# Kernel optimization log

Measured on AMD Instinct MI355X. Metric: run time of the kernel, lower is better.

## Reference

```python
import jax, jax.numpy as jnp
import numpy as np

NEG_SLOPE = 0.2  # PyG GATv2Conv default leaky_relu slope
N_NODES = 50000
N_EDGES = 800000
F_IN = 128
HID = 32
HEADS = 4
OUT_HEADS = 1
N_CLS = 16
MLP_HID = 128


def topk_mask(score, dst, k, num_nodes):
    """Boolean mask [E,H]: True where edge score is among top-k for its destination."""
    E = score.shape[0]
    counts = jnp.zeros((num_nodes,), jnp.int32).at[dst].add(1)
    starts = jnp.cumsum(counts) - counts  # first sorted index of each dst segment

    def one_head(s):
        o1 = jnp.argsort(-s)                       # sort by score desc
        o2 = jnp.argsort(dst[o1], stable=True)     # stable sort by dst -> (dst asc, score desc)
        perm = o1[o2]
        rank = jnp.arange(E) - starts[dst[perm]]   # rank within dst segment
        return jnp.zeros((E,), bool).at[perm].set(rank < k)

    return jax.vmap(one_head, in_axes=1, out_axes=1)(score)


def masked_segment_softmax(score, mask, dst, num_nodes):
    neg = jnp.where(mask, score, -jnp.inf)
    m = jax.ops.segment_max(neg, dst, num_segments=num_nodes)
    m = jnp.where(jnp.isfinite(m), m, 0.0)
    ex = jnp.where(mask, jnp.exp(score - m[dst]), 0.0)
    s = jax.ops.segment_sum(ex, dst, num_segments=num_nodes)
    return ex / (s[dst] + 1e-16)


def gatv2_topk(x, edge_index, k, Wl, Wr, att, b, heads, out_c, concat, num_nodes):
    src, dst = edge_index[0], edge_index[1]
    xl = (x @ Wl).reshape(num_nodes, heads, out_c)
    xr = (x @ Wr).reshape(num_nodes, heads, out_c)
    h = xl[src] + xr[dst]                                   # [E,H,C]
    e = jnp.einsum('ehc,hc->eh', jax.nn.leaky_relu(h, NEG_SLOPE), att)  # [E,H]
    keep = topk_mask(e, dst, k, num_nodes)
    alpha = masked_segment_softmax(e, keep, dst, num_nodes)       # top-k attention
    alpha_n = masked_segment_softmax(e, ~keep, dst, num_nodes)    # truncated (noise) attention
    msg = xl[src]                                                  # [E,H,C]
    out = jax.ops.segment_sum(alpha[..., None] * msg, dst, num_segments=num_nodes)
    noise = jax.ops.segment_sum(alpha_n[..., None] * msg, dst, num_segments=num_nodes)
    if concat:
        out = out.reshape(num_nodes, heads * out_c)
        noise = noise.reshape(num_nodes, heads * out_c)
    else:
        out = out.mean(axis=1)
        noise = noise.mean(axis=1)
    return out + b, noise + b


def setup_inputs() -> dict:
    key = jax.random.key(0)
    ks = jax.random.split(key, 14)
    s = 0.1
    x = jax.random.normal(ks[0], (N_NODES, F_IN), jnp.float32)
    edge_index = jax.random.randint(ks[1], (2, N_EDGES), 0, N_NODES, dtype=jnp.int64)
    return {
        'x': x,
        'edge_index': edge_index,
        'attn_topk': 8,
        'Wl1': jax.random.normal(ks[2], (F_IN, HEADS * HID), jnp.float32) * s,
        'Wr1': jax.random.normal(ks[3], (F_IN, HEADS * HID), jnp.float32) * s,
        'att1': jax.random.normal(ks[4], (HEADS, HID), jnp.float32) * s,
        'b1': jnp.zeros((HEADS * HID,), jnp.float32),
        'Wl2': jax.random.normal(ks[5], (HEADS * HID, OUT_HEADS * N_CLS), jnp.float32) * s,
        'Wr2': jax.random.normal(ks[6], (HEADS * HID, OUT_HEADS * N_CLS), jnp.float32) * s,
        'att2': jax.random.normal(ks[7], (OUT_HEADS, N_CLS), jnp.float32) * s,
        'b2': jnp.zeros((N_CLS,), jnp.float32),
        'lin1_w': jax.random.normal(ks[8], (HEADS * HID, MLP_HID), jnp.float32) * s,
        'lin1_b': jnp.zeros((MLP_HID,), jnp.float32),
        'lin2_w': jax.random.normal(ks[9], (MLP_HID, N_CLS), jnp.float32) * s,
        'lin2_b': jnp.zeros((N_CLS,), jnp.float32),
    }


def reference(x, edge_index, attn_topk, Wl1, Wr1, att1, b1, Wl2, Wr2, att2, b2,
              lin1_w, lin1_b, lin2_w, lin2_b):
    # eval mode: dropout is identity
    h, noise1 = gatv2_topk(x, edge_index, attn_topk, Wl1, Wr1, att1, b1,
                           HEADS, HID, True, N_NODES)
    h = jax.nn.elu(h)
    n1 = jax.nn.elu(noise1 @ lin1_w + lin1_b) @ lin2_w + lin2_b
    out, noise2 = gatv2_topk(h, edge_index, attn_topk, Wl2, Wr2, att2, b2,
                             OUT_HEADS, N_CLS, False, N_NODES)
    return (jax.nn.log_softmax(out, axis=1),
            jax.nn.log_softmax(n1, axis=1),
            jax.nn.log_softmax(noise2, axis=1))
```

## Files before the change

kernel.cpp:

```cpp
#include <hip/hip_runtime.h>
#include <math.h>

#define NN 50000
#define NE 800000
#define FIN 128
#define HEADS 4
#define HID 32
#define D1 128
#define NCLS 16
#define NEG 0.2f
#define NINF (-3.402823466e38f)
#define CAP 64
#define SB 256
#define NSB ((NN + SB - 1) / SB)

typedef unsigned long long ull;
typedef __attribute__((ext_vector_type(8))) short bf16x8;
typedef __attribute__((ext_vector_type(4))) float f32x4;

__device__ __forceinline__ short f2bf(float v) {
  unsigned u = __float_as_uint(v);
  unsigned r = (u + 0x7fffu + ((u >> 16) & 1u)) >> 16;
  return (short)r;
}

__global__ void k_count(const int* __restrict__ dst, int* __restrict__ counts) {
  int j = blockIdx.x * 256 + threadIdx.x;
  if (j < NE) atomicAdd(&counts[dst[j]], 1);
}

__global__ void k_scanA(const int* __restrict__ counts, int* __restrict__ bsum) {
  int b = blockIdx.x, t = threadIdx.x;
  int idx = b * SB + t;
  int v = idx < NN ? counts[idx] : 0;
  __shared__ int ws[4];
#pragma unroll
  for (int o = 1; o <= 32; o <<= 1) v += __shfl_xor(v, o, 64);
  if ((t & 63) == 0) ws[t >> 6] = v;
  __syncthreads();
  if (t == 0) bsum[b] = ws[0] + ws[1] + ws[2] + ws[3];
}

__global__ void k_scanB(const int* __restrict__ bsum, int* __restrict__ boff) {
  int t = threadIdx.x;
  int v = t < NSB ? bsum[t] : 0;
  __shared__ int tmp[256];
  tmp[t] = v;
  __syncthreads();
  for (int o = 1; o < 256; o <<= 1) {
    int u = t >= o ? tmp[t - o] : 0;
    __syncthreads();
    tmp[t] += u;
    __syncthreads();
  }
  if (t < NSB) boff[t] = tmp[t] - v;
}

__global__ void k_scanC(const int* __restrict__ counts, const int* __restrict__ boff,
                        int* __restrict__ starts, int* __restrict__ cursor) {
  int b = blockIdx.x, t = threadIdx.x;
  int idx = b * SB + t;
  int v = idx < NN ? counts[idx] : 0;
  __shared__ int tmp[256];
  tmp[t] = v;
  __syncthreads();
  for (int o = 1; o < 256; o <<= 1) {
    int u = t >= o ? tmp[t - o] : 0;
    __syncthreads();
    tmp[t] += u;
    __syncthreads();
  }
  int ex = tmp[t] - v + boff[b];
  if (idx < NN) { starts[idx] = ex; cursor[idx] = ex; }
}

__global__ void k_scatter(const int* __restrict__ src, const int* __restrict__ dst,
                          int* __restrict__ cursor, int* __restrict__ eperm,
                          int* __restrict__ sperm) {
  int j = blockIdx.x * 256 + threadIdx.x;
  if (j < NE) {
    int p = atomicAdd(&cursor[dst[j]], 1);
    eperm[p] = j;
    sperm[p] = src[j];
  }
}

template <int BM, int BN, int BK, int TM, int TN, int ACT>
__global__ __launch_bounds__(256) void k_gemm2(
    const float* __restrict__ A, const float* __restrict__ B1,
    const float* __restrict__ B2, int N1, int s1, int s2,
    const float* __restrict__ bias, float* __restrict__ C, int M, int N, int K) {
  constexpr int NT = (BM / TM) * (BN / TN);
  static_assert(NT == 256, "block must be 256 threads");
  static_assert(TM % 4 == 0 && TN % 4 == 0, "float4 fragments");
  __shared__ float As[BK][BM + 4];
  __shared__ float Bs[BK][BN];
  int tid = threadIdx.x;
  int bm = blockIdx.y * BM, bn = blockIdx.x * BN;
  constexpr int TX = BN / TN;
  int tn = (tid % TX) * TN;
  int tm = (tid / TX) * TM;
  float acc[TM][TN];
#pragma unroll
  for (int i = 0; i < TM; i++)
#pragma unroll
    for (int j = 0; j < TN; j++) acc[i][j] = 0.f;

  for (int k0 = 0; k0 < K; k0 += BK) {
    constexpr int AV = BM * BK / 4;
    for (int i = tid; i < AV; i += NT) {
      int r = i / (BK / 4);
      int c4 = (i % (BK / 4)) * 4;
      float4 v = make_float4(0.f, 0.f, 0.f, 0.f);
      int gr = bm + r;
      if (gr < M) v = *(const float4*)(A + (size_t)gr * K + k0 + c4);
      As[c4 + 0][r] = v.x; As[c4 + 1][r] = v.y; As[c4 + 2][r] = v.z; As[c4 + 3][r] = v.w;
    }
    constexpr int BV = BK * BN / 4;
    for (int i = tid; i < BV; i += NT) {
      int r = i / (BN / 4), c4 = (i % (BN / 4)) * 4;
      int gc = bn + c4, gk = k0 + r;
      float4 v = (gc < N1) ? *(const float4*)(B1 + (size_t)gk * s1 + gc)
                           : *(const float4*)(B2 + (size_t)gk * s2 + (gc - N1));
      Bs[r][c4 + 0] = v.x; Bs[r][c4 + 1] = v.y; Bs[r][c4 + 2] = v.z; Bs[r][c4 + 3] = v.w;
    }
    __syncthreads();
#pragma unroll
    for (int kk = 0; kk < BK; kk++) {
      float ra[TM], rb[TN];
#pragma unroll
      for (int i = 0; i < TM; i += 4)
        *(float4*)&ra[i] = *(const float4*)&As[kk][tm + i];
#pragma unroll
      for (int j = 0; j < TN; j += 4)
        *(float4*)&rb[j] = *(const float4*)&Bs[kk][tn + j];
#pragma unroll
      for (int i = 0; i < TM; i++)
#pragma unroll
        for (int j = 0; j < TN; j++) acc[i][j] += ra[i] * rb[j];
    }
    __syncthreads();
  }
#pragma unroll
  for (int i = 0; i < TM; i++) {
    int gr = bm + tm + i;
    if (gr >= M) continue;
#pragma unroll
    for (int j = 0; j < TN; j += 4) {
      float4 v;
      v.x = acc[i][j + 0]; v.y = acc[i][j + 1]; v.z = acc[i][j + 2]; v.w = acc[i][j + 3];
      if (bias) {
        v.x += bias[bn + tn + j + 0]; v.y += bias[bn + tn + j + 1];
        v.z += bias[bn + tn + j + 2]; v.w += bias[bn + tn + j + 3];
      }
      if (ACT == 1) {
        v.x = v.x > 0.f ? v.x : expm1f(v.x);
        v.y = v.y > 0.f ? v.y : expm1f(v.y);
        v.z = v.z > 0.f ? v.z : expm1f(v.z);
        v.w = v.w > 0.f ? v.w : expm1f(v.w);
      }
      *(float4*)(C + (size_t)gr * N + bn + tn + j) = v;
    }
  }
}

__global__ void k_cvtw(const float* __restrict__ l1w, const float* __restrict__ l2w,
                       short* __restrict__ w1t, short* __restrict__ w2t) {
  int t = blockIdx.x * 256 + threadIdx.x;
  if (t < 128 * 128) {
    int n = t >> 7, k = t & 127;
    w1t[t] = f2bf(l1w[k * 128 + n]);
  }
  if (t < 16 * 128) {
    int n = t >> 7, k = t & 127;
    w2t[t] = f2bf(l2w[k * 16 + n]);
  }
}

__global__ __launch_bounds__(256) void k_mlp1(
    const short* __restrict__ A, const short* __restrict__ BT,
    const float* __restrict__ bias, short* __restrict__ C) {
  int wv = threadIdx.x >> 6, lane = threadIdx.x & 63;
  int m0 = (blockIdx.x * 4 + wv) * 16;
  int quad = lane >> 4;
  int mr = m0 + (lane & 15);
  bool mok = mr < NN;
  bf16x8 afr[4];
#pragma unroll
  for (int kt = 0; kt < 4; kt++) {
    bf16x8 z = {0, 0, 0, 0, 0, 0, 0, 0};
    afr[kt] = mok ? *(const bf16x8*)(A + (size_t)mr * 128 + kt * 32 + quad * 8) : z;
  }
#pragma unroll
  for (int nt = 0; nt < 8; nt++) {
    f32x4 acc = {0.f, 0.f, 0.f, 0.f};
    int nc = nt * 16 + (lane & 15);
#pragma unroll
    for (int kt = 0; kt < 4; kt++) {
      bf16x8 bfr = *(const bf16x8*)(BT + (size_t)nc * 128 + kt * 32 + quad * 8);
      acc = __builtin_amdgcn_mfma_f32_16x16x32_bf16(afr[kt], bfr, acc, 0, 0, 0);
    }
    float bval = bias[nc];
#pragma unroll
    for (int r = 0; r < 4; r++) {
      int row = m0 + quad * 4 + r;
      if (row < NN) {
        float v = acc[r] + bval;
        v = v > 0.f ? v : expm1f(v);
        C[(size_t)row * 128 + nc] = f2bf(v);
      }
    }
  }
}

__global__ __launch_bounds__(256) void k_mlp2(
    const short* __restrict__ A, const short* __restrict__ BT,
    const float* __restrict__ bias, float* __restrict__ out) {
  int wv = threadIdx.x >> 6, lane = threadIdx.x & 63;
  int m0 = (blockIdx.x * 4 + wv) * 16;
  int quad = lane >> 4, col = lane & 15;
  int mr = m0 + col;
  bool mok = mr < NN;
  f32x4 acc = {0.f, 0.f, 0.f, 0.f};
#pragma unroll
  for (int kt = 0; kt < 4; kt++) {
    bf16x8 z = {0, 0, 0, 0, 0, 0, 0, 0};
    bf16x8 afr = mok ? *(const bf16x8*)(A + (size_t)mr * 128 + kt * 32 + quad * 8) : z;
    bf16x8 bfr = *(const bf16x8*)(BT + (size_t)col * 128 + kt * 32 + quad * 8);
    acc = __builtin_amdgcn_mfma_f32_16x16x32_bf16(afr, bfr, acc, 0, 0, 0);
  }
  float bval = bias[col];
#pragma unroll
  for (int r = 0; r < 4; r++) {
    float v = acc[r] + bval;
    float m = v;
#pragma unroll
    for (int o = 1; o <= 8; o <<= 1) m = fmaxf(m, __shfl_xor(m, o, 64));
    float e = __expf(v - m), s = e;
#pragma unroll
    for (int o = 1; o <= 8; o <<= 1) s += __shfl_xor(s, o, 64);
    int row = m0 + quad * 4 + r;
    if (row < NN) out[(size_t)row * NCLS + col] = v - (m + logf(s));
  }
}

__device__ __forceinline__ unsigned fkey(float f) {
  unsigned u = __float_as_uint(f);
  return u ^ (((int)u >> 31) | 0x80000000u);
}

__global__ __launch_bounds__(256) void k_fused1(
    const float* __restrict__ xlr, const float* __restrict__ att,
    const int* __restrict__ sperm, const int* __restrict__ eperm,
    const int* __restrict__ starts, const int* __restrict__ counts,
    const int* __restrict__ kptr, const float* __restrict__ bias,
    float* __restrict__ hout, short* __restrict__ nout) {
  __shared__ float sc[4][CAP][4];
  __shared__ ull keys[4][4][CAP + 1];
  int w = threadIdx.x >> 6;
  int l = threadIdx.x & 63;
  int d = blockIdx.x * 4 + w;
  if (d >= NN) return;
  int st = starts[d];
  int deg = counts[d];
  if (deg > CAP) deg = CAP;
  int k = kptr[0];

  int srcreg = 0, idreg = 0x7fffffff;
  if (l < deg) { srcreg = sperm[st + l]; idreg = eperm[st + l]; }

  int h2 = l >> 5, li = l & 31;
  int headq = li >> 3;
  float4 xrv = *(const float4*)(xlr + (size_t)d * 256 + 128 + 4 * li);
  float4 attv = *(const float4*)(att + 4 * li);
  float4 b1v = *(const float4*)(bias + 4 * li);

  float4 xc[8];
#pragma unroll
  for (int j = 0; j < 8; j++) xc[j] = make_float4(0.f, 0.f, 0.f, 0.f);

#pragma unroll
  for (int Q = 0; Q < 16; Q += 8) {
    if (Q < deg) {
      int rr[4]; float4 xv[4]; float pp[4]; bool vv[4];
#pragma unroll
      for (int j = 0; j < 4; j++) {
        rr[j] = Q + 2 * j + h2;
        int s = __shfl(srcreg, rr[j]);
        vv[j] = rr[j] < deg;
        xv[j] = make_float4(0.f, 0.f, 0.f, 0.f);
        if (vv[j]) xv[j] = *(const float4*)(xlr + (size_t)s * 256 + 4 * li);
        xc[Q / 2 + j] = xv[j];
      }
#pragma unroll
      for (int j = 0; j < 4; j++) {
        float a, p = 0.f;
        a = xv[j].x + xrv.x; p += fmaxf(a, NEG * a) * attv.x;
        a = xv[j].y + xrv.y; p += fmaxf(a, NEG * a) * attv.y;
        a = xv[j].z + xrv.z; p += fmaxf(a, NEG * a) * attv.z;
        a = xv[j].w + xrv.w; p += fmaxf(a, NEG * a) * attv.w;
        pp[j] = p;
      }
#pragma unroll
      for (int o = 1; o <= 4; o <<= 1) {
#pragma unroll
        for (int j = 0; j < 4; j++) pp[j] += __shfl_xor(pp[j], o, 64);
      }
      if ((li & 7) == 0) {
#pragma unroll
        for (int j = 0; j < 4; j++)
          if (vv[j]) sc[w][rr[j]][headq] = pp[j];
      }
    }
  }
  for (int q = 16; q < deg; q += 8) {
    int rr[4]; float4 xv[4]; float pp[4]; bool vv[4];
#pragma unroll
    for (int j = 0; j < 4; j++) {
      rr[j] = q + 2 * j + h2;
      int s = __shfl(srcreg, rr[j]);
      vv[j] = rr[j] < deg;
      xv[j] = make_float4(0.f, 0.f, 0.f, 0.f);
      if (vv[j]) xv[j] = *(const float4*)(xlr + (size_t)s * 256 + 4 * li);
    }
#pragma unroll
    for (int j = 0; j < 4; j++) {
      float a, p = 0.f;
      a = xv[j].x + xrv.x; p += fmaxf(a, NEG * a) * attv.x;
      a = xv[j].y + xrv.y; p += fmaxf(a, NEG * a) * attv.y;
      a = xv[j].z + xrv.z; p += fmaxf(a, NEG * a) * attv.z;
      a = xv[j].w + xrv.w; p += fmaxf(a, NEG * a) * attv.w;
      pp[j] = p;
    }
#pragma unroll
    for (int o = 1; o <= 4; o <<= 1) {
#pragma unroll
      for (int j = 0; j < 4; j++) pp[j] += __shfl_xor(pp[j], o, 64);
    }
    if ((li & 7) == 0) {
#pragma unroll
      for (int j = 0; j < 4; j++)
        if (vv[j]) sc[w][rr[j]][headq] = pp[j];
    }
  }

  int hh = l >> 4, ii = l & 15;
  float sv[4]; bool val[4]; ull mkey[4]; int rank[4];
#pragma unroll
  for (int j = 0; j < 4; j++) {
    int q = j * 16 + ii;
    val[j] = q < deg;
    sv[j] = val[j] ? sc[w][q][hh] : NINF;
    int bid = __shfl(idreg, q);
    mkey[j] = val[j] ? (((ull)fkey(sv[j]) << 32) | (unsigned)~bid) : 0ull;
    rank[j] = 0;
    if (val[j]) keys[w][hh][q] = mkey[j];
  }
  int nch = (deg + 15) >> 4;
  const ull* kp = keys[w][hh];
  if (nch == 1) {
    int r0 = 0;
    for (int p = 0; p < deg; p++) r0 += kp[p] > mkey[0];
    rank[0] = r0;
  } else if (nch == 2) {
    int r0 = 0, r1 = 0;
    for (int p = 0; p < deg; p++) {
      ull bk = kp[p];
      r0 += bk > mkey[0]; r1 += bk > mkey[1];
    }
    rank[0] = r0; rank[1] = r1;
  } else {
    for (int p = 0; p < deg; p++) {
      ull bk = kp[p];
#pragma unroll
      for (int j = 0; j < 4; j++) rank[j] += bk > mkey[j];
    }
  }
  bool kept[4];
#pragma unroll
  for (int j = 0; j < 4; j++) kept[j] = val[j] && (rank[j] < k);

  float mk = fmaxf(fmaxf(sv[0], sv[1]), fmaxf(sv[2], sv[3]));
  float mn = NINF;
#pragma unroll
  for (int j = 0; j < 4; j++) mn = fmaxf(mn, kept[j] ? NINF : sv[j]);
#pragma unroll
  for (int o = 1; o <= 8; o <<= 1) {
    mk = fmaxf(mk, __shfl_xor(mk, o, 64));
    mn = fmaxf(mn, __shfl_xor(mn, o, 64));
  }
  float ek[4], en[4], sk = 0.f, sn = 0.f;
#pragma unroll
  for (int j = 0; j < 4; j++) {
    ek[j] = kept[j] ? __expf(sv[j] - mk) : 0.f;
    en[j] = (val[j] && !kept[j]) ? __expf(sv[j] - mn) : 0.f;
    sk += ek[j]; sn += en[j];
  }
#pragma unroll
  for (int o = 1; o <= 8; o <<= 1) {
    sk += __shfl_xor(sk, o, 64);
    sn += __shfl_xor(sn, o, 64);
  }
  float ik = 1.f / (sk + 1e-16f), inn = 1.f / (sn + 1e-16f);
#pragma unroll
  for (int j = 0; j < 4; j++) {
    if (val[j]) sc[w][j * 16 + ii][hh] = kept[j] ? ek[j] * ik : -(en[j] * inn);
  }

  float4 ao = make_float4(0.f, 0.f, 0.f, 0.f), an = ao;
#pragma unroll
  for (int j = 0; j < 8; j++) {
    int r = 2 * j + h2;
    if (r < deg) {
      float wv = sc[w][r][headq];
      float pw = fmaxf(wv, 0.f), nw = pw - wv;
      float4 xv = xc[j];
      ao.x += pw * xv.x; ao.y += pw * xv.y; ao.z += pw * xv.z; ao.w += pw * xv.w;
      an.x += nw * xv.x; an.y += nw * xv.y; an.z += nw * xv.z; an.w += nw * xv.w;
    }
  }
  for (int q = 16; q < deg; q += 4) {
    int r0 = q + h2, r1 = q + 2 + h2;
    int s0 = __shfl(srcreg, r0), s1 = __shfl(srcreg, r1);
    if (r0 < deg) {
      float wv = sc[w][r0][headq];
      float pw = fmaxf(wv, 0.f), nw = pw - wv;
      float4 xv = *(const float4*)(xlr + (size_t)s0 * 256 + 4 * li);
      ao.x += pw * xv.x; ao.y += pw * xv.y; ao.z += pw * xv.z; ao.w += pw * xv.w;
      an.x += nw * xv.x; an.y += nw * xv.y; an.z += nw * xv.z; an.w += nw * xv.w;
    }
    if (r1 < deg) {
      float wv = sc[w][r1][headq];
      float pw = fmaxf(wv, 0.f), nw = pw - wv;
      float4 xv = *(const float4*)(xlr + (size_t)s1 * 256 + 4 * li);
      ao.x += pw * xv.x; ao.y += pw * xv.y; ao.z += pw * xv.z; ao.w += pw * xv.w;
      an.x += nw * xv.x; an.y += nw * xv.y; an.z += nw * xv.z; an.w += nw * xv.w;
    }
  }
  ao.x += __shfl_xor(ao.x, 32, 64); ao.y += __shfl_xor(ao.y, 32, 64);
  ao.z += __shfl_xor(ao.z, 32, 64); ao.w += __shfl_xor(ao.w, 32, 64);
  an.x += __shfl_xor(an.x, 32, 64); an.y += __shfl_xor(an.y, 32, 64);
  an.z += __shfl_xor(an.z, 32, 64); an.w += __shfl_xor(an.w, 32, 64);
  if (h2 == 0) {
    float4 vo;
    vo.x = ao.x + b1v.x; vo.y = ao.y + b1v.y; vo.z = ao.z + b1v.z; vo.w = ao.w + b1v.w;
    vo.x = vo.x > 0.f ? vo.x : expm1f(vo.x);
    vo.y = vo.y > 0.f ? vo.y : expm1f(vo.y);
    vo.z = vo.z > 0.f ? vo.z : expm1f(vo.z);
    vo.w = vo.w > 0.f ? vo.w : expm1f(vo.w);
    *(float4*)(hout + (size_t)d * D1 + 4 * li) = vo;
  } else {
    short4 vn;
    vn.x = f2bf(an.x + b1v.x); vn.y = f2bf(an.y + b1v.y);
    vn.z = f2bf(an.z + b1v.z); vn.w = f2bf(an.w + b1v.w);
    *(short4*)(nout + (size_t)d * D1 + 4 * li) = vn;
  }
}

__global__ __launch_bounds__(256) void k_fused2(
    const float* __restrict__ xlr, const float* __restrict__ att,
    const int* __restrict__ sperm, const int* __restrict__ eperm,
    const int* __restrict__ starts, const int* __restrict__ counts,
    const int* __restrict__ kptr, const float* __restrict__ bias,
    float* __restrict__ out0, float* __restrict__ out1) {
  __shared__ float sc[4][CAP];
  __shared__ ull keys[4][CAP];
  int w = threadIdx.x >> 6;
  int l = threadIdx.x & 63;
  int d = blockIdx.x * 4 + w;
  if (d >= NN) return;
  int st = starts[d];
  int deg = counts[d];
  if (deg > CAP) deg = CAP;
  int k = kptr[0];

  int srcreg = 0, idreg = 0x7fffffff;
  if (l < deg) { srcreg = sperm[st + l]; idreg = eperm[st + l]; }

  int g = l >> 4, li = l & 15;
  float xrv = xlr[(size_t)d * 32 + 16 + li];
  float attv = att[li];
  float bv2 = bias[li];

  float xc[8];
#pragma unroll
  for (int j = 0; j < 8; j++) xc[j] = 0.f;

#pragma unroll
  for (int Q = 0; Q < 32; Q += 8) {
    if (Q < deg) {
      int r0 = Q + g, r1 = Q + 4 + g;
      int s0 = __shfl(srcreg, r0), s1 = __shfl(srcreg, r1);
      float x0 = (r0 < deg) ? xlr[(size_t)s0 * 32 + li] : 0.f;
      float x1 = (r1 < deg) ? xlr[(size_t)s1 * 32 + li] : 0.f;
      xc[Q / 4] = x0; xc[Q / 4 + 1] = x1;
      float a0 = x0 + xrv, a1 = x1 + xrv;
      float p0 = fmaxf(a0, NEG * a0) * attv;
      float p1 = fmaxf(a1, NEG * a1) * attv;
#pragma unroll
      for (int o = 1; o <= 8; o <<= 1) {
        p0 += __shfl_xor(p0, o, 64);
        p1 += __shfl_xor(p1, o, 64);
      }
      if (li == 0) {
        if (r0 < deg) sc[w][r0] = p0;
        if (r1 < deg) sc[w][r1] = p1;
      }
    }
  }
  for (int q = 32; q < deg; q += 8) {
    int r0 = q + g, r1 = q + 4 + g;
    int s0 = __shfl(srcreg, r0), s1 = __shfl(srcreg, r1);
    float x0 = (r0 < deg) ? xlr[(size_t)s0 * 32 + li] : 0.f;
    float x1 = (r1 < deg) ? xlr[(size_t)s1 * 32 + li] : 0.f;
    float a0 = x0 + xrv, a1 = x1 + xrv;
    float p0 = fmaxf(a0, NEG * a0) * attv;
    float p1 = fmaxf(a1, NEG * a1) * attv;
#pragma unroll
    for (int o = 1; o <= 8; o <<= 1) {
      p0 += __shfl_xor(p0, o, 64);
      p1 += __shfl_xor(p1, o, 64);
    }
    if (li == 0) {
      if (r0 < deg) sc[w][r0] = p0;
      if (r1 < deg) sc[w][r1] = p1;
    }
  }

  float sv = (l < deg) ? sc[w][l] : NINF;
  ull mk64 = (l < deg) ? (((ull)fkey(sv) << 32) | (unsigned)~idreg) : 0ull;
  if (l < deg) keys[w][l] = mk64;
  int rank = 0;
  for (int p = 0; p < deg; p++) rank += keys[w][p] > mk64;
  bool kept = (l < deg) && (rank < k);

  float mk = sv, mn = kept ? NINF : sv;
#pragma unroll
  for (int o = 1; o <= 32; o <<= 1) {
    mk = fmaxf(mk, __shfl_xor(mk, o, 64));
    mn = fmaxf(mn, __shfl_xor(mn, o, 64));
  }
  float ek = kept ? __expf(sv - mk) : 0.f;
  float en = ((l < deg) && !kept) ? __expf(sv - mn) : 0.f;
  float sk = ek, sn = en;
#pragma unroll
  for (int o = 1; o <= 32; o <<= 1) {
    sk += __shfl_xor(sk, o, 64);
    sn += __shfl_xor(sn, o, 64);
  }
  if (l < deg) sc[w][l] = kept ? ek / (sk + 1e-16f) : -(en / (sn + 1e-16f));

  float ao = 0.f, an = 0.f;
#pragma unroll
  for (int j = 0; j < 8; j++) {
    int r = 4 * j + g;
    if (r < deg) {
      float wv = sc[w][r];
      float pw = fmaxf(wv, 0.f), nw = pw - wv;
      ao += pw * xc[j]; an += nw * xc[j];
    }
  }
  for (int q = 32; q < deg; q += 4) {
    int r = q + g;
    int s = __shfl(srcreg, r);
    if (r < deg) {
      float wv = sc[w][r];
      float pw = fmaxf(wv, 0.f), nw = pw - wv;
      float xv = xlr[(size_t)s * 32 + li];
      ao += pw * xv; an += nw * xv;
    }
  }
  ao += __shfl_xor(ao, 16, 64); ao += __shfl_xor(ao, 32, 64);
  an += __shfl_xor(an, 16, 64); an += __shfl_xor(an, 32, 64);
  float vo = ao + bv2, vn = an + bv2;
  float mo = vo, mv = vn;
#pragma unroll
  for (int o = 1; o <= 8; o <<= 1) {
    mo = fmaxf(mo, __shfl_xor(mo, o, 64));
    mv = fmaxf(mv, __shfl_xor(mv, o, 64));
  }
  float eo = __expf(vo - mo), ev = __expf(vn - mv);
#pragma unroll
  for (int o = 1; o <= 8; o <<= 1) {
    eo += __shfl_xor(eo, o, 64);
    ev += __shfl_xor(ev, o, 64);
  }
  if (g == 0) out0[(size_t)d * NCLS + li] = vo - (mo + logf(eo));
  if (g == 1) out1[(size_t)d * NCLS + li] = vn - (mv + logf(ev));
}

extern "C" void kernel_launch(void* const* d_in, const int* in_sizes, int n_in,
                              void* d_out, int out_size, void* d_ws, size_t ws_size,
                              hipStream_t stream) {
  (void)in_sizes; (void)n_in; (void)out_size; (void)ws_size;
  const float* x    = (const float*)d_in[0];
  const int*   ei   = (const int*)d_in[1];
  const int*   kptr = (const int*)d_in[2];
  const float* Wl1  = (const float*)d_in[3];
  const float* Wr1  = (const float*)d_in[4];
  const float* att1 = (const float*)d_in[5];
  const float* b1   = (const float*)d_in[6];
  const float* Wl2  = (const float*)d_in[7];
  const float* Wr2  = (const float*)d_in[8];
  const float* att2 = (const float*)d_in[9];
  const float* b2   = (const float*)d_in[10];
  const float* l1w  = (const float*)d_in[11];
  const float* l1b  = (const float*)d_in[12];
  const float* l2w  = (const float*)d_in[13];
  const float* l2b  = (const float*)d_in[14];
  const int* srcv = ei;
  const int* dstv = ei + NE;

  char* wp = (char*)d_ws;
  auto alloc = [&](size_t n) { char* p = wp; wp += (n + 255) & ~(size_t)255; return p; };
  float* xlr1   = (float*)alloc((size_t)NN * 256 * 4);
  float* hbuf   = (float*)alloc((size_t)NN * D1 * 4);
  short* noise1 = (short*)alloc((size_t)NN * D1 * 2);
  short* t1     = (short*)alloc((size_t)NN * D1 * 2);
  float* xlr2   = (float*)alloc((size_t)NN * 32 * 4);
  short* w1t    = (short*)alloc((size_t)128 * 128 * 2);
  short* w2t    = (short*)alloc((size_t)16 * 128 * 2);
  int* counts = (int*)alloc((size_t)NN * 4);
  int* starts = (int*)alloc((size_t)NN * 4);
  int* cursor = (int*)alloc((size_t)NN * 4);
  int* eperm  = (int*)alloc((size_t)NE * 4);
  int* sperm  = (int*)alloc((size_t)NE * 4);
  int* bsum   = (int*)alloc((size_t)NSB * 4);
  int* boff   = (int*)alloc((size_t)NSB * 4);

  hipMemsetAsync(counts, 0, (size_t)NN * 4, stream);
  k_count<<<(NE + 255) / 256, 256, 0, stream>>>(dstv, counts);
  k_scanA<<<NSB, 256, 0, stream>>>(counts, bsum);
  k_scanB<<<1, 256, 0, stream>>>(bsum, boff);
  k_scanC<<<NSB, 256, 0, stream>>>(counts, boff, starts, cursor);
  k_scatter<<<(NE + 255) / 256, 256, 0, stream>>>(srcv, dstv, cursor, eperm, sperm);

  k_cvtw<<<64, 256, 0, stream>>>(l1w, l2w, w1t, w2t);

  k_gemm2<64, 128, 32, 4, 8, 0><<<dim3(2, (NN + 63) / 64), 256, 0, stream>>>(
      x, Wl1, Wr1, 128, 128, 128, nullptr, xlr1, NN, 256, FIN);

  k_fused1<<<(NN + 3) / 4, 256, 0, stream>>>(xlr1, att1, sperm, eperm,
                                             starts, counts, kptr, b1, hbuf, noise1);

  float* o = (float*)d_out;

  k_mlp1<<<(NN + 63) / 64, 256, 0, stream>>>(noise1, w1t, l1b, t1);
  k_mlp2<<<(NN + 63) / 64, 256, 0, stream>>>(t1, w2t, l2b, o + (size_t)NN * NCLS);

  k_gemm2<128, 32, 32, 4, 4, 0><<<dim3(1, (NN + 127) / 128), 256, 0, stream>>>(
      hbuf, Wl2, Wr2, 16, 16, 16, nullptr, xlr2, NN, 32, D1);

  k_fused2<<<(NN + 3) / 4, 256, 0, stream>>>(xlr2, att2, sperm, eperm, starts,
                                             counts, kptr, b2, o,
                                             o + (size_t)2 * NN * NCLS);
}
```

Measured before the change: 424.6 us.

## Fuse noise MLP kernels and split layer-2 projections into separate compact buffers

Merges the two noise-branch MLP kernels into one, keeping the bf16 hidden activation in shared memory instead of writing and rereading a global buffer. The layer-2 GEMM now writes its left and right projections to separate 16-wide arrays, so the gather in the second attention kernel reads a denser 64-byte row per source node. This removes a global round trip and one launch, and may improve cache use for the random gathers. The fused MLP uses extra shared memory per block, which could lower occupancy slightly.

```diff
diff --git a/kernel.cpp b/kernel.cpp
--- a/kernel.cpp
+++ b/kernel.cpp
@@ -89,7 +89,8 @@
 __global__ __launch_bounds__(256) void k_gemm2(
     const float* __restrict__ A, const float* __restrict__ B1,
     const float* __restrict__ B2, int N1, int s1, int s2,
-    const float* __restrict__ bias, float* __restrict__ C, int M, int N, int K) {
+    const float* __restrict__ bias, float* __restrict__ C1, int so1,
+    float* __restrict__ C2, int so2, int M, int N, int K) {
   constexpr int NT = (BM / TM) * (BN / TN);
   static_assert(NT == 256, "block must be 256 threads");
   static_assert(TM % 4 == 0 && TN % 4 == 0, "float4 fragments");
@@ -159,7 +160,9 @@
         v.z = v.z > 0.f ? v.z : expm1f(v.z);
         v.w = v.w > 0.f ? v.w : expm1f(v.w);
       }
-      *(float4*)(C + (size_t)gr * N + bn + tn + j) = v;
+      int gc = bn + tn + j;
+      if (gc < N1) *(float4*)(C1 + (size_t)gr * so1 + gc) = v;
+      else         *(float4*)(C2 + (size_t)gr * so2 + (gc - N1)) = v;
     }
   }
 }
@@ -177,62 +180,50 @@
   }
 }
 
-__global__ __launch_bounds__(256) void k_mlp1(
-    const short* __restrict__ A, const short* __restrict__ BT,
-    const float* __restrict__ bias, short* __restrict__ C) {
-  int wv = threadIdx.x >> 6, lane = threadIdx.x & 63;
-  int m0 = (blockIdx.x * 4 + wv) * 16;
-  int quad = lane >> 4;
-  int mr = m0 + (lane & 15);
-  bool mok = mr < NN;
-  bf16x8 afr[4];
-#pragma unroll
-  for (int kt = 0; kt < 4; kt++) {
-    bf16x8 z = {0, 0, 0, 0, 0, 0, 0, 0};
-    afr[kt] = mok ? *(const bf16x8*)(A + (size_t)mr * 128 + kt * 32 + quad * 8) : z;
-  }
-#pragma unroll
-  for (int nt = 0; nt < 8; nt++) {
-    f32x4 acc = {0.f, 0.f, 0.f, 0.f};
-    int nc = nt * 16 + (lane & 15);
-#pragma unroll
-    for (int kt = 0; kt < 4; kt++) {
-      bf16x8 bfr = *(const bf16x8*)(BT + (size_t)nc * 128 + kt * 32 + quad * 8);
-      acc = __builtin_amdgcn_mfma_f32_16x16x32_bf16(afr[kt], bfr, acc, 0, 0, 0);
-    }
-    float bval = bias[nc];
-#pragma unroll
-    for (int r = 0; r < 4; r++) {
-      int row = m0 + quad * 4 + r;
-      if (row < NN) {
-        float v = acc[r] + bval;
-        v = v > 0.f ? v : expm1f(v);
-        C[(size_t)row * 128 + nc] = f2bf(v);
-      }
-    }
-  }
-}
-
-__global__ __launch_bounds__(256) void k_mlp2(
-    const short* __restrict__ A, const short* __restrict__ BT,
-    const float* __restrict__ bias, float* __restrict__ out) {
+__global__ __launch_bounds__(256) void k_mlp(
+    const short* __restrict__ A, const short* __restrict__ W1T,
+    const float* __restrict__ b1, const short* __restrict__ W2T,
+    const float* __restrict__ b2, float* __restrict__ out) {
+  __shared__ short tls[4][16][136];
   int wv = threadIdx.x >> 6, lane = threadIdx.x & 63;
   int m0 = (blockIdx.x * 4 + wv) * 16;
   int quad = lane >> 4, col = lane & 15;
   int mr = m0 + col;
   bool mok = mr < NN;
-  f32x4 acc = {0.f, 0.f, 0.f, 0.f};
+  bf16x8 z = {0, 0, 0, 0, 0, 0, 0, 0};
+  bf16x8 afr[4];
+#pragma unroll
+  for (int kt = 0; kt < 4; kt++)
+    afr[kt] = mok ? *(const bf16x8*)(A + (size_t)mr * 128 + kt * 32 + quad * 8) : z;
+#pragma unroll
+  for (int nt = 0; nt < 8; nt++) {
+    f32x4 acc = {0.f, 0.f, 0.f, 0.f};
+    int nc = nt * 16 + col;
+#pragma unroll
+    for (int kt = 0; kt < 4; kt++) {
+      bf16x8 bfr = *(const bf16x8*)(W1T + (size_t)nc * 128 + kt * 32 + quad * 8);
+      acc = __builtin_amdgcn_mfma_f32_16x16x32_bf16(afr[kt], bfr, acc, 0, 0, 0);
+    }
+    float bval = b1[nc];
+#pragma unroll
+    for (int r = 0; r < 4; r++) {
+      float v = acc[r] + bval;
+      v = v > 0.f ? v : expm1f(v);
+      tls[wv][quad * 4 + r][nc] = f2bf(v);
+    }
+  }
+  __syncthreads();
+  f32x4 acc2 = {0.f, 0.f, 0.f, 0.f};
 #pragma unroll
   for (int kt = 0; kt < 4; kt++) {
-    bf16x8 z = {0, 0, 0, 0, 0, 0, 0, 0};
-    bf16x8 afr = mok ? *(const bf16x8*)(A + (size_t)mr * 128 + kt * 32 + quad * 8) : z;
-    bf16x8 bfr = *(const bf16x8*)(BT + (size_t)col * 128 + kt * 32 + quad * 8);
-    acc = __builtin_amdgcn_mfma_f32_16x16x32_bf16(afr, bfr, acc, 0, 0, 0);
-  }
-  float bval = bias[col];
+    bf16x8 afr2 = *(const bf16x8*)&tls[wv][col][kt * 32 + quad * 8];
+    bf16x8 bfr = *(const bf16x8*)(W2T + (size_t)col * 128 + kt * 32 + quad * 8);
+    acc2 = __builtin_amdgcn_mfma_f32_16x16x32_bf16(afr2, bfr, acc2, 0, 0, 0);
+  }
+  float bval = b2[col];
 #pragma unroll
   for (int r = 0; r < 4; r++) {
-    float v = acc[r] + bval;
+    float v = acc2[r] + bval;
     float m = v;
 #pragma unroll
     for (int o = 1; o <= 8; o <<= 1) m = fmaxf(m, __shfl_xor(m, o, 64));
@@ -458,11 +449,12 @@
 }
 
 __global__ __launch_bounds__(256) void k_fused2(
-    const float* __restrict__ xlr, const float* __restrict__ att,
-    const int* __restrict__ sperm, const int* __restrict__ eperm,
-    const int* __restrict__ starts, const int* __restrict__ counts,
-    const int* __restrict__ kptr, const float* __restrict__ bias,
-    float* __restrict__ out0, float* __restrict__ out1) {
+    const float* __restrict__ xl2, const float* __restrict__ xr2,
+    const float* __restrict__ att, const int* __restrict__ sperm,
+    const int* __restrict__ eperm, const int* __restrict__ starts,
+    const int* __restrict__ counts, const int* __restrict__ kptr,
+    const float* __restrict__ bias, float* __restrict__ out0,
+    float* __restrict__ out1) {
   __shared__ float sc[4][CAP];
   __shared__ ull keys[4][CAP];
   int w = threadIdx.x >> 6;
@@ -478,7 +470,7 @@
   if (l < deg) { srcreg = sperm[st + l]; idreg = eperm[st + l]; }
 
   int g = l >> 4, li = l & 15;
-  float xrv = xlr[(size_t)d * 32 + 16 + li];
+  float xrv = xr2[(size_t)d * 16 + li];
   float attv = att[li];
   float bv2 = bias[li];
 
@@ -491,8 +483,8 @@
     if (Q < deg) {
       int r0 = Q + g, r1 = Q + 4 + g;
       int s0 = __shfl(srcreg, r0), s1 = __shfl(srcreg, r1);
-      float x0 = (r0 < deg) ? xlr[(size_t)s0 * 32 + li] : 0.f;
-      float x1 = (r1 < deg) ? xlr[(size_t)s1 * 32 + li] : 0.f;
+      float x0 = (r0 < deg) ? xl2[(size_t)s0 * 16 + li] : 0.f;
+      float x1 = (r1 < deg) ? xl2[(size_t)s1 * 16 + li] : 0.f;
       xc[Q / 4] = x0; xc[Q / 4 + 1] = x1;
       float a0 = x0 + xrv, a1 = x1 + xrv;
       float p0 = fmaxf(a0, NEG * a0) * attv;
@@ -511,8 +503,8 @@
   for (int q = 32; q < deg; q += 8) {
     int r0 = q + g, r1 = q + 4 + g;
     int s0 = __shfl(srcreg, r0), s1 = __shfl(srcreg, r1);
-    float x0 = (r0 < deg) ? xlr[(size_t)s0 * 32 + li] : 0.f;
-    float x1 = (r1 < deg) ? xlr[(size_t)s1 * 32 + li] : 0.f;
+    float x0 = (r0 < deg) ? xl2[(size_t)s0 * 16 + li] : 0.f;
+    float x1 = (r1 < deg) ? xl2[(size_t)s1 * 16 + li] : 0.f;
     float a0 = x0 + xrv, a1 = x1 + xrv;
     float p0 = fmaxf(a0, NEG * a0) * attv;
     float p1 = fmaxf(a1, NEG * a1) * attv;
@@ -566,7 +558,7 @@
     if (r < deg) {
       float wv = sc[w][r];
       float pw = fmaxf(wv, 0.f), nw = pw - wv;
-      float xv = xlr[(size_t)s * 32 + li];
+      float xv = xl2[(size_t)s * 16 + li];
       ao += pw * xv; an += nw * xv;
     }
   }
@@ -616,8 +608,8 @@
   float* xlr1   = (float*)alloc((size_t)NN * 256 * 4);
   float* hbuf   = (float*)alloc((size_t)NN * D1 * 4);
   short* noise1 = (short*)alloc((size_t)NN * D1 * 2);
-  short* t1     = (short*)alloc((size_t)NN * D1 * 2);
-  float* xlr2   = (float*)alloc((size_t)NN * 32 * 4);
+  float* xl2    = (float*)alloc((size_t)NN * 16 * 4);
+  float* xr2    = (float*)alloc((size_t)NN * 16 * 4);
   short* w1t    = (short*)alloc((size_t)128 * 128 * 2);
   short* w2t    = (short*)alloc((size_t)16 * 128 * 2);
   int* counts = (int*)alloc((size_t)NN * 4);
@@ -638,20 +630,20 @@
   k_cvtw<<<64, 256, 0, stream>>>(l1w, l2w, w1t, w2t);
 
   k_gemm2<64, 128, 32, 4, 8, 0><<<dim3(2, (NN + 63) / 64), 256, 0, stream>>>(
-      x, Wl1, Wr1, 128, 128, 128, nullptr, xlr1, NN, 256, FIN);
+      x, Wl1, Wr1, 128, 128, 128, nullptr, xlr1, 256, xlr1 + 128, 256, NN, 256, FIN);
 
   k_fused1<<<(NN + 3) / 4, 256, 0, stream>>>(xlr1, att1, sperm, eperm,
                                              starts, counts, kptr, b1, hbuf, noise1);
 
   float* o = (float*)d_out;
 
-  k_mlp1<<<(NN + 63) / 64, 256, 0, stream>>>(noise1, w1t, l1b, t1);
-  k_mlp2<<<(NN + 63) / 64, 256, 0, stream>>>(t1, w2t, l2b, o + (size_t)NN * NCLS);
+  k_mlp<<<(NN + 63) / 64, 256, 0, stream>>>(noise1, w1t, l1b, w2t, l2b,
+                                            o + (size_t)NN * NCLS);
 
   k_gemm2<128, 32, 32, 4, 4, 0><<<dim3(1, (NN + 127) / 128), 256, 0, stream>>>(
-      hbuf, Wl2, Wr2, 16, 16, 16, nullptr, xlr2, NN, 32, D1);
-
-  k_fused2<<<(NN + 3) / 4, 256, 0, stream>>>(xlr2, att2, sperm, eperm, starts,
+      hbuf, Wl2, Wr2, 16, 16, 16, nullptr, xl2, 16, xr2, 16, NN, 32, D1);
+
+  k_fused2<<<(NN + 3) / 4, 256, 0, stream>>>(xl2, xr2, att2, sperm, eperm, starts,
                                              counts, kptr, b2, o,
                                              o + (size_t)2 * NN * NCLS);
 }
```

Result: slower. 436.9 us (+2.9%).
